# Performance work log

Measured on AMD Instinct MI355X. Metric: run time of the kernel, lower is better.

Reference implementation:

```python
import jax, jax.numpy as jnp
import numpy as np

N = 20000          # nodes (= masked tokens M, node_ids = arange)
E = 320000         # edges
D_H = 256          # hidden_channels
D_Z = 256          # node_channels
D_A = 256          # attn_channels
D_M = 256          # mlp_hidden_channels
V = 512            # predictor vocab size


def setup_inputs() -> dict:
    key = jax.random.key(0)
    ks = jax.random.split(key, 10)

    def lin(k, fan_in, fan_out):
        return jax.random.normal(k, (fan_in, fan_out), jnp.float32) / np.sqrt(fan_in)

    h_mask = jax.random.normal(ks[0], (N, D_H), jnp.float32)
    z = jax.random.normal(ks[1], (N, D_Z), jnp.float32)
    edge_index = jax.random.randint(ks[2], (2, E), 0, N, dtype=jnp.int32)
    node_ids = jnp.arange(N, dtype=jnp.int32)
    # Pairing of (masked token, edge): with node_ids = arange(N), every edge's
    # dst is a masked node, so masked_idx = dst and edge_idx = arange(E).
    masked_idx = edge_index[1]
    edge_idx = jnp.arange(E, dtype=jnp.int32)
    return {
        "h_mask": h_mask,
        "z": z,
        "Wq": lin(ks[3], D_Z, D_A), "bq": jnp.zeros((D_A,), jnp.float32),
        "Wk": lin(ks[4], D_Z, D_A), "bk": jnp.zeros((D_A,), jnp.float32),
        "W1": lin(ks[5], D_Z, D_M), "b1": jnp.zeros((D_M,), jnp.float32),
        "W2": lin(ks[6], D_M, D_H), "b2": jnp.zeros((D_H,), jnp.float32),
        "Wpred": lin(ks[7], D_H, V), "bpred": jnp.zeros((V,), jnp.float32),
        "edge_index": edge_index,
        "node_ids": node_ids,
        "masked_idx": masked_idx,
        "edge_idx": edge_idx,
    }


def reference(h_mask, z, Wq, bq, Wk, bk, W1, b1, W2, b2, Wpred, bpred,
              edge_index, node_ids, masked_idx, edge_idx):
    src = edge_index[0]
    # Node-level projections (N x D), computed once then gathered per pair.
    q = z @ Wq + bq                      # [N, D_A]
    k = z @ Wk + bk                      # [N, D_A]

    center_nodes = jnp.take(node_ids, masked_idx, axis=0)   # [P]
    neighbor_nodes = jnp.take(src, edge_idx, axis=0)        # [P]

    q_i = jnp.take(q, center_nodes, axis=0)                 # [P, D_A]
    k_j = jnp.take(k, neighbor_nodes, axis=0)               # [P, D_A]
    a_ij = jax.nn.sigmoid(jnp.sum(q_i * k_j, axis=-1, keepdims=True))  # [P, 1]

    h_i = jnp.take(h_mask, masked_idx, axis=0)              # [P, D_H]
    z_j = jnp.take(z, neighbor_nodes, axis=0)               # [P, D_Z]
    g_zj = jax.nn.relu(z_j @ W1 + b1) @ W2 + b2             # [P, D_H]

    h_tilde = a_ij * h_i + (1.0 - a_ij) * g_zj              # [P, D_H]
    edge_logits = h_tilde @ Wpred + bpred                   # [P, V]
    return edge_logits, masked_idx
```

## Files before the change

### kernel.cpp

```cpp
#include <hip/hip_runtime.h>
#include <hip/hip_bf16.h>

typedef __attribute__((ext_vector_type(8))) short s16x8;
typedef __attribute__((ext_vector_type(4))) float f32x4;
typedef __attribute__((ext_vector_type(2))) float f32x2;

__device__ inline unsigned int f2bf(float f) {
    union { float f; unsigned int i; } v;
    v.f = f;
    return (v.i + 0x7FFFu + ((v.i >> 16) & 1u)) >> 16;
}
__device__ inline unsigned char f2fp8(float v) {
    const int p = __builtin_amdgcn_cvt_pk_fp8_f32(v, v, 0, false);
    return (unsigned char)(p & 0xFF);
}

__global__ __launch_bounds__(256) void prep_w(
    const float* __restrict__ Wq, const float* __restrict__ Wk,
    const float* __restrict__ W1, const float* __restrict__ W2,
    const float* __restrict__ Wp,
    const float* __restrict__ bq, const float* __restrict__ bk,
    const float* __restrict__ b1,
    unsigned short* __restrict__ Wtqkt, unsigned short* __restrict__ Wt2,
    unsigned short* __restrict__ Wtp, float* __restrict__ bqkt)
{
    const int tid = threadIdx.x;
    int b = blockIdx.x;
    if (b < 1024) {
        const int w = b >> 8;
        const int i = (b & 255) * 256 + tid;
        const int k = i >> 8, j = i & 255;
        const float* W = (w == 0) ? Wq : (w == 1) ? Wk : (w == 2) ? W1 : W2;
        unsigned short* dst = (w == 3) ? Wt2 : (Wtqkt + w * 65536);
        dst[j * 256 + k] = (unsigned short)f2bf(W[i]);
        return;
    }
    b -= 1024;
    if (b < 512) {
        const int i = b * 256 + tid;
        const int k = i >> 9, j = i & 511;
        Wtp[(size_t)j * 256 + k] = (unsigned short)f2bf(Wp[i]);
        return;
    }
    b -= 512;
    {
        const int i = b * 256 + tid;
        bqkt[i] = (i < 256) ? bq[i] : (i < 512) ? bk[i - 256] : b1[i - 512];
    }
}

struct GemmJob {
    const void* A;
    const unsigned short* Wt;
    const float* bias;
    void* out1;
    void* out2;
    int Nout;
    int split;
    int relu_lo, relu_hi;
    int a_f32;
    int fp8_1, fp8_2;
};

__device__ inline void job_store(const GemmJob& J, int row, int col, float v, int M) {
    if (row >= M) return;
    if (J.bias) v += J.bias[col];
    if (col >= J.relu_lo && col < J.relu_hi) v = fmaxf(v, 0.0f);
    const bool lo = (col < J.split);
    void* o = lo ? J.out1 : J.out2;
    const int stride = lo ? J.split : (J.Nout - J.split);
    const int cc = lo ? col : col - J.split;
    const int f8 = lo ? J.fp8_1 : J.fp8_2;
    if (f8) ((unsigned char*)o)[(size_t)row * stride + cc] = f2fp8(v);
    else    ((unsigned short*)o)[(size_t)row * stride + cc] = (unsigned short)f2bf(v);
}

__global__ __launch_bounds__(256) void gemm_multi(
    GemmJob j0, GemmJob j1, int M)
{
    __shared__ __align__(16) char smem[65536];
    char* ldsA = smem;
    char* ldsB = smem + 32768;
    const GemmJob J = (blockIdx.y == 0) ? j0 : j1;

    const int tid  = threadIdx.x;
    const int wid  = tid >> 6, lane = tid & 63;
    const int wr   = wid >> 1, wc = wid & 1;
    const int r0   = blockIdx.x * 64;
    const int swz  = (lane & 7) << 4;

    if (J.a_f32) {
        const float* Af = (const float*)J.A;
        for (int i = tid; i < 2048; i += 256) {
            const int row = i >> 5, off = i & 31;
            const int gr = r0 + row;
            uint4 v = make_uint4(0, 0, 0, 0);
            if (gr < M) {
                const float4 a = *(const float4*)(Af + (size_t)gr * 256 + off * 8);
                const float4 c = *(const float4*)(Af + (size_t)gr * 256 + off * 8 + 4);
                v.x = f2bf(a.x) | (f2bf(a.y) << 16);
                v.y = f2bf(a.z) | (f2bf(a.w) << 16);
                v.z = f2bf(c.x) | (f2bf(c.y) << 16);
                v.w = f2bf(c.z) | (f2bf(c.w) << 16);
            }
            const int b = (row * 512 + off * 16) ^ ((row & 7) << 4);
            *(uint4*)(ldsA + b) = v;
        }
    } else {
        const unsigned short* Ab = (const unsigned short*)J.A;
        for (int i = tid; i < 2048; i += 256) {
            const int row = i >> 5, off = i & 31;
            const int gr = r0 + row;
            uint4 v = make_uint4(0, 0, 0, 0);
            if (gr < M) v = *(const uint4*)(Ab + (size_t)gr * 256 + off * 8);
            const int b = (row * 512 + off * 16) ^ ((row & 7) << 4);
            *(uint4*)(ldsA + b) = v;
        }
    }

    const int ro = lane & 15, ko = (lane >> 4) * 16;
    const int baseA0 = (wr * 32 +  0 + ro) * 512 + ko;
    const int baseA1 = (wr * 32 + 16 + ro) * 512 + ko;
    const int baseB0 = (wc * 32 +  0 + ro) * 512 + ko;
    const int baseB1 = (wc * 32 + 16 + ro) * 512 + ko;

    const int nchunks = J.Nout >> 6;
    for (int c = 0; c < nchunks; ++c) {
        const int j0c = c << 6;
        for (int i = tid; i < 2048; i += 256) {
            const int row = i >> 5, off = i & 31;
            const uint4 v = *(const uint4*)(J.Wt + (size_t)(j0c + row) * 256 + off * 8);
            const int b = (row * 512 + off * 16) ^ ((row & 7) << 4);
            *(uint4*)(ldsB + b) = v;
        }
        __syncthreads();

        f32x4 acc00 = {0,0,0,0}, acc01 = {0,0,0,0}, acc10 = {0,0,0,0}, acc11 = {0,0,0,0};
#pragma unroll
        for (int kk = 0; kk < 8; ++kk) {
            const int kb = kk * 64;
            const s16x8 a0 = *(const s16x8*)(ldsA + ((baseA0 + kb) ^ swz));
            const s16x8 a1 = *(const s16x8*)(ldsA + ((baseA1 + kb) ^ swz));
            const s16x8 b0 = *(const s16x8*)(ldsB + ((baseB0 + kb) ^ swz));
            const s16x8 b1 = *(const s16x8*)(ldsB + ((baseB1 + kb) ^ swz));
            acc00 = __builtin_amdgcn_mfma_f32_16x16x32_bf16(a0, b0, acc00, 0, 0, 0);
            acc01 = __builtin_amdgcn_mfma_f32_16x16x32_bf16(a0, b1, acc01, 0, 0, 0);
            acc10 = __builtin_amdgcn_mfma_f32_16x16x32_bf16(a1, b0, acc10, 0, 0, 0);
            acc11 = __builtin_amdgcn_mfma_f32_16x16x32_bf16(a1, b1, acc11, 0, 0, 0);
        }

        const int colb = j0c + wc * 32;
        const int rb0 = r0 + wr * 32 + (lane >> 4) * 4;
        const int rb1 = rb0 + 16;
#pragma unroll
        for (int r = 0; r < 4; ++r) {
            job_store(J, rb0 + r, colb + ro,      acc00[r], M);
            job_store(J, rb0 + r, colb + 16 + ro, acc01[r], M);
            job_store(J, rb1 + r, colb + ro,      acc10[r], M);
            job_store(J, rb1 + r, colb + 16 + ro, acc11[r], M);
        }
        __syncthreads();
    }
}

__global__ __launch_bounds__(256) void edge_fused(
    const unsigned char* __restrict__ qkb,
    const unsigned char* __restrict__ hp, const unsigned char* __restrict__ gp,
    const float* __restrict__ bpred,
    const int* __restrict__ edge_src, const int* __restrict__ node_ids,
    const int* __restrict__ masked_idx, const int* __restrict__ edge_idx,
    float* __restrict__ out, int P)
{
    const int wave = threadIdx.x >> 6;
    const int lane = threadIdx.x & 63;
    const int e = blockIdx.x * 4 + wave;
    if (e >= P) return;

    const int mi = masked_idx[e];
    const int c  = node_ids[mi];
    const int s  = edge_src[edge_idx[e]];

    const unsigned int qw = *(const unsigned int*)(qkb + (size_t)c * 512 + lane * 4);
    const unsigned int kw = *(const unsigned int*)(qkb + (size_t)s * 512 + 256 + lane * 4);
    const f32x2 q01 = __builtin_amdgcn_cvt_pk_f32_fp8(qw, false);
    const f32x2 q23 = __builtin_amdgcn_cvt_pk_f32_fp8(qw, true);
    const f32x2 k01 = __builtin_amdgcn_cvt_pk_f32_fp8(kw, false);
    const f32x2 k23 = __builtin_amdgcn_cvt_pk_f32_fp8(kw, true);
    float dot = q01.x * k01.x + q01.y * k01.y + q23.x * k23.x + q23.y * k23.y;
#pragma unroll
    for (int off = 32; off; off >>= 1) dot += __shfl_xor(dot, off, 64);

    const float a = 1.0f / (1.0f + expf(-dot));
    const float oma = 1.0f - a;

    const uint2 hv = *(const uint2*)(hp + (size_t)c * 512 + lane * 8);
    const uint2 gv = *(const uint2*)(gp + (size_t)s * 512 + lane * 8);
    const float4 bp0 = *(const float4*)&bpred[lane * 8];
    const float4 bp1 = *(const float4*)&bpred[lane * 8 + 4];

    const f32x2 h0 = __builtin_amdgcn_cvt_pk_f32_fp8(hv.x, false);
    const f32x2 h1 = __builtin_amdgcn_cvt_pk_f32_fp8(hv.x, true);
    const f32x2 h2 = __builtin_amdgcn_cvt_pk_f32_fp8(hv.y, false);
    const f32x2 h3 = __builtin_amdgcn_cvt_pk_f32_fp8(hv.y, true);
    const f32x2 g0 = __builtin_amdgcn_cvt_pk_f32_fp8(gv.x, false);
    const f32x2 g1 = __builtin_amdgcn_cvt_pk_f32_fp8(gv.x, true);
    const f32x2 g2 = __builtin_amdgcn_cvt_pk_f32_fp8(gv.y, false);
    const f32x2 g3 = __builtin_amdgcn_cvt_pk_f32_fp8(gv.y, true);

    f32x4 r0, r1;
    r0[0] = fmaf(a, h0.x, fmaf(oma, g0.x, bp0.x));
    r0[1] = fmaf(a, h0.y, fmaf(oma, g0.y, bp0.y));
    r0[2] = fmaf(a, h1.x, fmaf(oma, g1.x, bp0.z));
    r0[3] = fmaf(a, h1.y, fmaf(oma, g1.y, bp0.w));
    r1[0] = fmaf(a, h2.x, fmaf(oma, g2.x, bp1.x));
    r1[1] = fmaf(a, h2.y, fmaf(oma, g2.y, bp1.y));
    r1[2] = fmaf(a, h3.x, fmaf(oma, g3.x, bp1.z));
    r1[3] = fmaf(a, h3.y, fmaf(oma, g3.y, bp1.w));

    float* dst = &out[(size_t)e * 512 + lane * 8];
    __builtin_nontemporal_store(r0, (f32x4*)dst);
    __builtin_nontemporal_store(r1, (f32x4*)(dst + 4));

    if (lane == 0) {
        __builtin_nontemporal_store((float)mi, &out[(size_t)P * 512 + e]);
    }
}

extern "C" void kernel_launch(void* const* d_in, const int* in_sizes, int n_in,
                              void* d_out, int out_size, void* d_ws, size_t ws_size,
                              hipStream_t stream) {
    const float* h_mask = (const float*)d_in[0];
    const float* z      = (const float*)d_in[1];
    const float* Wq     = (const float*)d_in[2];
    const float* bq     = (const float*)d_in[3];
    const float* Wk     = (const float*)d_in[4];
    const float* bk     = (const float*)d_in[5];
    const float* W1     = (const float*)d_in[6];
    const float* b1     = (const float*)d_in[7];
    const float* W2     = (const float*)d_in[8];
    const float* b2     = (const float*)d_in[9];
    const float* Wpred  = (const float*)d_in[10];
    const float* bpred  = (const float*)d_in[11];
    const int* edge_index = (const int*)d_in[12];
    const int* node_ids   = (const int*)d_in[13];
    const int* masked_idx = (const int*)d_in[14];
    const int* edge_idx   = (const int*)d_in[15];

    const int N = in_sizes[13];
    const int P = in_sizes[14];

    unsigned char*  qkb   = (unsigned char*)d_ws;
    unsigned char*  gpb   = qkb + (size_t)N * 512;
    unsigned char*  hpb   = gpb + (size_t)N * 512;
    unsigned short* tb    = (unsigned short*)(hpb + (size_t)N * 512);
    unsigned short* gb    = tb  + (size_t)N * 256;
    unsigned short* Wtqkt = gb  + (size_t)N * 256;
    unsigned short* Wt2   = Wtqkt + 196608;
    unsigned short* Wtp   = Wt2   + 65536;
    float*          bqkt  = (float*)(Wtp + 131072);

    const dim3 blk(256);
    const int gb64 = (N + 63) / 64;
    const int eb   = (P + 3) / 4;

    prep_w<<<dim3(1024 + 512 + 3), blk, 0, stream>>>(
        Wq, Wk, W1, W2, Wpred, bq, bk, b1, Wtqkt, Wt2, Wtp, bqkt);

    GemmJob a0 = { z,      Wtqkt, bqkt,    qkb, tb,      768, 512, 512, 768, 1, 1, 0 };
    GemmJob a1 = { h_mask, Wtp,   nullptr, hpb, nullptr, 512, 512, 0,   0,   1, 1, 0 };
    gemm_multi<<<dim3(gb64, 2), blk, 0, stream>>>(a0, a1, N);

    GemmJob b0 = { tb, Wt2, b2, gb, nullptr, 256, 256, 0, 0, 0, 0, 0 };
    gemm_multi<<<dim3(gb64, 1), blk, 0, stream>>>(b0, b0, N);

    GemmJob c0 = { gb, Wtp, nullptr, gpb, nullptr, 512, 512, 0, 0, 0, 1, 0 };
    gemm_multi<<<dim3(gb64, 1), blk, 0, stream>>>(c0, c0, N);

    edge_fused<<<dim3(eb), blk, 0, stream>>>(qkb, hpb, gpb, bpred,
                                             edge_index, node_ids, masked_idx, edge_idx,
                                             (float*)d_out, P);
}
```

Before: 319.9 us.

## Counting-sort edges by center node before the fused edge kernel

Adds a counting sort (histogram, single-block scan, atomic scatter) that groups edges by their center node and packs each edge's indices into an int4 record. The edge kernel then walks edges in sorted order, so that q and h rows of the same center node are reused in cache and the index indirection is a single load. The cost is three extra small kernels, including a single-block serial scan over N, plus atomics and a 5 MB index buffer. Output writes still go to the original edge positions, so they become scattered.

```diff
diff --git a/kernel.cpp b/kernel.cpp
--- a/kernel.cpp
+++ b/kernel.cpp
@@ -22,7 +22,8 @@
     const float* __restrict__ bq, const float* __restrict__ bk,
     const float* __restrict__ b1,
     unsigned short* __restrict__ Wtqkt, unsigned short* __restrict__ Wt2,
-    unsigned short* __restrict__ Wtp, float* __restrict__ bqkt)
+    unsigned short* __restrict__ Wtp, float* __restrict__ bqkt,
+    int* __restrict__ counts, int N)
 {
     const int tid = threadIdx.x;
     int b = blockIdx.x;
@@ -43,10 +44,65 @@
         return;
     }
     b -= 512;
+    if (b < 3) {
+        const int i = b * 256 + tid;
+        bqkt[i] = (i < 256) ? bq[i] : (i < 512) ? bk[i - 256] : b1[i - 512];
+        return;
+    }
+    b -= 3;
     {
         const int i = b * 256 + tid;
-        bqkt[i] = (i < 256) ? bq[i] : (i < 512) ? bk[i - 256] : b1[i - 512];
-    }
+        if (i < N) counts[i] = 0;
+    }
+}
+
+__global__ __launch_bounds__(256) void sort_hist(
+    const int* __restrict__ node_ids, const int* __restrict__ masked_idx,
+    int* __restrict__ counts, int P)
+{
+    const int e = blockIdx.x * 256 + threadIdx.x;
+    if (e >= P) return;
+    const int c = node_ids[masked_idx[e]];
+    atomicAdd(&counts[c], 1);
+}
+
+__global__ __launch_bounds__(256) void sort_scan(
+    const int* __restrict__ counts, int* __restrict__ cursor, int N)
+{
+    __shared__ int part[256];
+    const int tid = threadIdx.x;
+    const int chunk = (N + 255) / 256;
+    const int lo = tid * chunk, hi = min(lo + chunk, N);
+
+    int ls = 0;
+    for (int i = lo; i < hi; ++i) ls += counts[i];
+    part[tid] = ls;
+    __syncthreads();
+    for (int off = 1; off < 256; off <<= 1) {
+        int v = (tid >= off) ? part[tid - off] : 0;
+        __syncthreads();
+        part[tid] += v;
+        __syncthreads();
+    }
+    int run = part[tid] - ls;
+    for (int i = lo; i < hi; ++i) {
+        cursor[i] = run;
+        run += counts[i];
+    }
+}
+
+__global__ __launch_bounds__(256) void sort_scatter(
+    const int* __restrict__ edge_src, const int* __restrict__ node_ids,
+    const int* __restrict__ masked_idx, const int* __restrict__ edge_idx,
+    int* __restrict__ cursor, int4* __restrict__ sorted, int P)
+{
+    const int e = blockIdx.x * 256 + threadIdx.x;
+    if (e >= P) return;
+    const int mi = masked_idx[e];
+    const int c  = node_ids[mi];
+    const int s  = edge_src[edge_idx[e]];
+    const int pos = atomicAdd(&cursor[c], 1);
+    sorted[pos] = make_int4(e, mi, c, s);
 }
 
 struct GemmJob {
@@ -163,22 +219,20 @@
     }
 }
 
-__global__ __launch_bounds__(256) void edge_fused(
+__global__ __launch_bounds__(256) void edge_sorted(
+    const int4* __restrict__ sorted,
     const unsigned char* __restrict__ qkb,
     const unsigned char* __restrict__ hp, const unsigned char* __restrict__ gp,
     const float* __restrict__ bpred,
-    const int* __restrict__ edge_src, const int* __restrict__ node_ids,
-    const int* __restrict__ masked_idx, const int* __restrict__ edge_idx,
     float* __restrict__ out, int P)
 {
     const int wave = threadIdx.x >> 6;
     const int lane = threadIdx.x & 63;
-    const int e = blockIdx.x * 4 + wave;
-    if (e >= P) return;
-
-    const int mi = masked_idx[e];
-    const int c  = node_ids[mi];
-    const int s  = edge_src[edge_idx[e]];
+    const int ep = blockIdx.x * 4 + wave;
+    if (ep >= P) return;
+
+    const int4 t = sorted[ep];
+    const int e = t.x, mi = t.y, c = t.z, s = t.w;
 
     const unsigned int qw = *(const unsigned int*)(qkb + (size_t)c * 512 + lane * 4);
     const unsigned int kw = *(const unsigned int*)(qkb + (size_t)s * 512 + 256 + lane * 4);
@@ -258,13 +312,23 @@
     unsigned short* Wt2   = Wtqkt + 196608;
     unsigned short* Wtp   = Wt2   + 65536;
     float*          bqkt  = (float*)(Wtp + 131072);
+    int*            counts = (int*)(bqkt + 768);
+    int*            cursor = counts + N;
+    int4*           sorted = (int4*)(cursor + N);
 
     const dim3 blk(256);
     const int gb64 = (N + 63) / 64;
     const int eb   = (P + 3) / 4;
-
-    prep_w<<<dim3(1024 + 512 + 3), blk, 0, stream>>>(
-        Wq, Wk, W1, W2, Wpred, bq, bk, b1, Wtqkt, Wt2, Wtp, bqkt);
+    const int pb   = (P + 255) / 256;
+    const int nb   = (N + 255) / 256;
+
+    prep_w<<<dim3(1024 + 512 + 3 + nb), blk, 0, stream>>>(
+        Wq, Wk, W1, W2, Wpred, bq, bk, b1, Wtqkt, Wt2, Wtp, bqkt, counts, N);
+
+    sort_hist<<<dim3(pb), blk, 0, stream>>>(node_ids, masked_idx, counts, P);
+    sort_scan<<<dim3(1), blk, 0, stream>>>(counts, cursor, N);
+    sort_scatter<<<dim3(pb), blk, 0, stream>>>(edge_index, node_ids, masked_idx, edge_idx,
+                                               cursor, sorted, P);
 
     GemmJob a0 = { z,      Wtqkt, bqkt,    qkb, tb,      768, 512, 512, 768, 1, 1, 0 };
     GemmJob a1 = { h_mask, Wtp,   nullptr, hpb, nullptr, 512, 512, 0,   0,   1, 1, 0 };
@@ -276,7 +340,6 @@
     GemmJob c0 = { gb, Wtp, nullptr, gpb, nullptr, 512, 512, 0, 0, 0, 1, 0 };
     gemm_multi<<<dim3(gb64, 1), blk, 0, stream>>>(c0, c0, N);
 
-    edge_fused<<<dim3(eb), blk, 0, stream>>>(qkb, hpb, gpb, bpred,
-                                             edge_index, node_ids, masked_idx, edge_idx,
-                                             (float*)d_out, P);
-}
+    edge_sorted<<<dim3(eb), blk, 0, stream>>>(sorted, qkb, hpb, gpb, bpred,
+                                              (float*)d_out, P);
+}
```

New measurement: 457.6 us. +43.0%, slower.

## Fuse node-level GEMM chain into one kernel keeping MLP intermediates in LDS

Applied to the files above, without the earlier changes.

Replaces three gemm_multi launches with a single gemm_fused kernel. For z blocks it computes q/k, then the relu(zW1) tile is held in registers and written back into the LDS A tile. That tile feeds the W2 GEMM and then the Wpred projection, so the bf16 intermediates tb and gb never go to global memory. This removes two launches and the global round-trips of the intermediates, but the z-row blocks now do much more work than the h blocks, which risks load imbalance and higher register pressure.

```diff
diff --git a/kernel.cpp b/kernel.cpp
--- a/kernel.cpp
+++ b/kernel.cpp
@@ -49,48 +49,33 @@
     }
 }
 
-struct GemmJob {
-    const void* A;
-    const unsigned short* Wt;
-    const float* bias;
-    void* out1;
-    void* out2;
-    int Nout;
-    int split;
-    int relu_lo, relu_hi;
-    int a_f32;
-    int fp8_1, fp8_2;
-};
-
-__device__ inline void job_store(const GemmJob& J, int row, int col, float v, int M) {
-    if (row >= M) return;
-    if (J.bias) v += J.bias[col];
-    if (col >= J.relu_lo && col < J.relu_hi) v = fmaxf(v, 0.0f);
-    const bool lo = (col < J.split);
-    void* o = lo ? J.out1 : J.out2;
-    const int stride = lo ? J.split : (J.Nout - J.split);
-    const int cc = lo ? col : col - J.split;
-    const int f8 = lo ? J.fp8_1 : J.fp8_2;
-    if (f8) ((unsigned char*)o)[(size_t)row * stride + cc] = f2fp8(v);
-    else    ((unsigned short*)o)[(size_t)row * stride + cc] = (unsigned short)f2bf(v);
-}
-
-__global__ __launch_bounds__(256) void gemm_multi(
-    GemmJob j0, GemmJob j1, int M)
+__global__ __launch_bounds__(256) void gemm_fused(
+    const float* __restrict__ z, const float* __restrict__ h,
+    const unsigned short* __restrict__ Wtqkt, const unsigned short* __restrict__ Wt2,
+    const unsigned short* __restrict__ Wtp,
+    const float* __restrict__ bqkt, const float* __restrict__ b2,
+    unsigned char* __restrict__ qkb, unsigned char* __restrict__ hpb,
+    unsigned char* __restrict__ gpb, int M)
 {
     __shared__ __align__(16) char smem[65536];
     char* ldsA = smem;
     char* ldsB = smem + 32768;
-    const GemmJob J = (blockIdx.y == 0) ? j0 : j1;
 
     const int tid  = threadIdx.x;
     const int wid  = tid >> 6, lane = tid & 63;
     const int wr   = wid >> 1, wc = wid & 1;
     const int r0   = blockIdx.x * 64;
     const int swz  = (lane & 7) << 4;
-
-    if (J.a_f32) {
-        const float* Af = (const float*)J.A;
+    const int ro   = lane & 15, ko = (lane >> 4) * 16;
+    const int lr0  = wr * 32 + (lane >> 4) * 4;
+    const int baseA0 = (wr * 32 +  0 + ro) * 512 + ko;
+    const int baseA1 = (wr * 32 + 16 + ro) * 512 + ko;
+    const int baseB0 = (wc * 32 +  0 + ro) * 512 + ko;
+    const int baseB1 = (wc * 32 + 16 + ro) * 512 + ko;
+
+    f32x4 a00, a01, a10, a11;
+
+    auto stageAf = [&](const float* Af) {
         for (int i = tid; i < 2048; i += 256) {
             const int row = i >> 5, off = i & 31;
             const int gr = r0 + row;
@@ -103,64 +88,112 @@
                 v.z = f2bf(c.x) | (f2bf(c.y) << 16);
                 v.w = f2bf(c.z) | (f2bf(c.w) << 16);
             }
-            const int b = (row * 512 + off * 16) ^ ((row & 7) << 4);
-            *(uint4*)(ldsA + b) = v;
-        }
-    } else {
-        const unsigned short* Ab = (const unsigned short*)J.A;
+            *(uint4*)(ldsA + ((row * 512 + off * 16) ^ ((row & 7) << 4))) = v;
+        }
+    };
+
+    auto chunk = [&](const unsigned short* Wt, int rowbase) {
         for (int i = tid; i < 2048; i += 256) {
             const int row = i >> 5, off = i & 31;
-            const int gr = r0 + row;
-            uint4 v = make_uint4(0, 0, 0, 0);
-            if (gr < M) v = *(const uint4*)(Ab + (size_t)gr * 256 + off * 8);
-            const int b = (row * 512 + off * 16) ^ ((row & 7) << 4);
-            *(uint4*)(ldsA + b) = v;
-        }
-    }
-
-    const int ro = lane & 15, ko = (lane >> 4) * 16;
-    const int baseA0 = (wr * 32 +  0 + ro) * 512 + ko;
-    const int baseA1 = (wr * 32 + 16 + ro) * 512 + ko;
-    const int baseB0 = (wc * 32 +  0 + ro) * 512 + ko;
-    const int baseB1 = (wc * 32 + 16 + ro) * 512 + ko;
-
-    const int nchunks = J.Nout >> 6;
-    for (int c = 0; c < nchunks; ++c) {
-        const int j0c = c << 6;
-        for (int i = tid; i < 2048; i += 256) {
-            const int row = i >> 5, off = i & 31;
-            const uint4 v = *(const uint4*)(J.Wt + (size_t)(j0c + row) * 256 + off * 8);
-            const int b = (row * 512 + off * 16) ^ ((row & 7) << 4);
-            *(uint4*)(ldsB + b) = v;
+            const uint4 v = *(const uint4*)(Wt + (size_t)(rowbase + row) * 256 + off * 8);
+            *(uint4*)(ldsB + ((row * 512 + off * 16) ^ ((row & 7) << 4))) = v;
         }
         __syncthreads();
-
-        f32x4 acc00 = {0,0,0,0}, acc01 = {0,0,0,0}, acc10 = {0,0,0,0}, acc11 = {0,0,0,0};
+        a00 = (f32x4){0,0,0,0}; a01 = (f32x4){0,0,0,0};
+        a10 = (f32x4){0,0,0,0}; a11 = (f32x4){0,0,0,0};
 #pragma unroll
         for (int kk = 0; kk < 8; ++kk) {
             const int kb = kk * 64;
-            const s16x8 a0 = *(const s16x8*)(ldsA + ((baseA0 + kb) ^ swz));
-            const s16x8 a1 = *(const s16x8*)(ldsA + ((baseA1 + kb) ^ swz));
-            const s16x8 b0 = *(const s16x8*)(ldsB + ((baseB0 + kb) ^ swz));
-            const s16x8 b1 = *(const s16x8*)(ldsB + ((baseB1 + kb) ^ swz));
-            acc00 = __builtin_amdgcn_mfma_f32_16x16x32_bf16(a0, b0, acc00, 0, 0, 0);
-            acc01 = __builtin_amdgcn_mfma_f32_16x16x32_bf16(a0, b1, acc01, 0, 0, 0);
-            acc10 = __builtin_amdgcn_mfma_f32_16x16x32_bf16(a1, b0, acc10, 0, 0, 0);
-            acc11 = __builtin_amdgcn_mfma_f32_16x16x32_bf16(a1, b1, acc11, 0, 0, 0);
-        }
-
-        const int colb = j0c + wc * 32;
-        const int rb0 = r0 + wr * 32 + (lane >> 4) * 4;
-        const int rb1 = rb0 + 16;
+            const s16x8 x0 = *(const s16x8*)(ldsA + ((baseA0 + kb) ^ swz));
+            const s16x8 x1 = *(const s16x8*)(ldsA + ((baseA1 + kb) ^ swz));
+            const s16x8 y0 = *(const s16x8*)(ldsB + ((baseB0 + kb) ^ swz));
+            const s16x8 y1 = *(const s16x8*)(ldsB + ((baseB1 + kb) ^ swz));
+            a00 = __builtin_amdgcn_mfma_f32_16x16x32_bf16(x0, y0, a00, 0, 0, 0);
+            a01 = __builtin_amdgcn_mfma_f32_16x16x32_bf16(x0, y1, a01, 0, 0, 0);
+            a10 = __builtin_amdgcn_mfma_f32_16x16x32_bf16(x1, y0, a10, 0, 0, 0);
+            a11 = __builtin_amdgcn_mfma_f32_16x16x32_bf16(x1, y1, a11, 0, 0, 0);
+        }
+    };
+
+    auto store_fp8 = [&](unsigned char* outb, int colbase, const float* bias) {
+        const int cb = colbase + wc * 32;
+        const float bs0 = bias ? bias[cb + ro] : 0.0f;
+        const float bs1 = bias ? bias[cb + 16 + ro] : 0.0f;
+        const int gr0 = r0 + lr0, gr1 = gr0 + 16;
 #pragma unroll
         for (int r = 0; r < 4; ++r) {
-            job_store(J, rb0 + r, colb + ro,      acc00[r], M);
-            job_store(J, rb0 + r, colb + 16 + ro, acc01[r], M);
-            job_store(J, rb1 + r, colb + ro,      acc10[r], M);
-            job_store(J, rb1 + r, colb + 16 + ro, acc11[r], M);
+            if (gr0 + r < M) {
+                outb[(size_t)(gr0 + r) * 512 + cb + ro]      = f2fp8(a00[r] + bs0);
+                outb[(size_t)(gr0 + r) * 512 + cb + 16 + ro] = f2fp8(a01[r] + bs1);
+            }
+            if (gr1 + r < M) {
+                outb[(size_t)(gr1 + r) * 512 + cb + ro]      = f2fp8(a10[r] + bs0);
+                outb[(size_t)(gr1 + r) * 512 + cb + 16 + ro] = f2fp8(a11[r] + bs1);
+            }
         }
         __syncthreads();
-    }
+    };
+
+    auto frag_to_ldsA = [&](const unsigned int* treg) {
+#pragma unroll
+        for (int tc = 0; tc < 4; ++tc) {
+            const int cb = tc * 64 + wc * 32;
+#pragma unroll
+            for (int r = 0; r < 4; ++r) {
+                const unsigned int w0 = treg[tc * 8 + r * 2];
+                const unsigned int w1 = treg[tc * 8 + r * 2 + 1];
+                const int row0 = lr0 + r, row1 = row0 + 16;
+                *(unsigned short*)(ldsA + ((row0 * 512 + (cb + ro) * 2)      ^ ((row0 & 7) << 4))) = (unsigned short)(w0 & 0xFFFFu);
+                *(unsigned short*)(ldsA + ((row0 * 512 + (cb + 16 + ro) * 2) ^ ((row0 & 7) << 4))) = (unsigned short)(w0 >> 16);
+                *(unsigned short*)(ldsA + ((row1 * 512 + (cb + ro) * 2)      ^ ((row1 & 7) << 4))) = (unsigned short)(w1 & 0xFFFFu);
+                *(unsigned short*)(ldsA + ((row1 * 512 + (cb + 16 + ro) * 2) ^ ((row1 & 7) << 4))) = (unsigned short)(w1 >> 16);
+            }
+        }
+    };
+
+    if (blockIdx.y == 1) {
+        stageAf(h);
+        for (int c = 0; c < 8; ++c) { chunk(Wtp, c * 64); store_fp8(hpb, c * 64, nullptr); }
+        return;
+    }
+
+    stageAf(z);
+    for (int c = 0; c < 8; ++c) { chunk(Wtqkt, c * 64); store_fp8(qkb, c * 64, bqkt); }
+
+    unsigned int treg[32];
+#pragma unroll
+    for (int tc = 0; tc < 4; ++tc) {
+        chunk(Wtqkt, 512 + tc * 64);
+        const int cb = tc * 64 + wc * 32;
+        const float bs0 = bqkt[512 + cb + ro];
+        const float bs1 = bqkt[512 + cb + 16 + ro];
+#pragma unroll
+        for (int r = 0; r < 4; ++r) {
+            treg[tc * 8 + r * 2]     = f2bf(fmaxf(a00[r] + bs0, 0.0f)) | (f2bf(fmaxf(a01[r] + bs1, 0.0f)) << 16);
+            treg[tc * 8 + r * 2 + 1] = f2bf(fmaxf(a10[r] + bs0, 0.0f)) | (f2bf(fmaxf(a11[r] + bs1, 0.0f)) << 16);
+        }
+        __syncthreads();
+    }
+    frag_to_ldsA(treg);
+    __syncthreads();
+
+#pragma unroll
+    for (int gc = 0; gc < 4; ++gc) {
+        chunk(Wt2, gc * 64);
+        const int cb = gc * 64 + wc * 32;
+        const float bs0 = b2[cb + ro];
+        const float bs1 = b2[cb + 16 + ro];
+#pragma unroll
+        for (int r = 0; r < 4; ++r) {
+            treg[gc * 8 + r * 2]     = f2bf(a00[r] + bs0) | (f2bf(a01[r] + bs1) << 16);
+            treg[gc * 8 + r * 2 + 1] = f2bf(a10[r] + bs0) | (f2bf(a11[r] + bs1) << 16);
+        }
+        __syncthreads();
+    }
+    frag_to_ldsA(treg);
+    __syncthreads();
+
+    for (int c = 0; c < 8; ++c) { chunk(Wtp, c * 64); store_fp8(gpb, c * 64, nullptr); }
 }
 
 __global__ __launch_bounds__(256) void edge_fused(
@@ -252,9 +285,7 @@
     unsigned char*  qkb   = (unsigned char*)d_ws;
     unsigned char*  gpb   = qkb + (size_t)N * 512;
     unsigned char*  hpb   = gpb + (size_t)N * 512;
-    unsigned short* tb    = (unsigned short*)(hpb + (size_t)N * 512);
-    unsigned short* gb    = tb  + (size_t)N * 256;
-    unsigned short* Wtqkt = gb  + (size_t)N * 256;
+    unsigned short* Wtqkt = (unsigned short*)(hpb + (size_t)N * 512);
     unsigned short* Wt2   = Wtqkt + 196608;
     unsigned short* Wtp   = Wt2   + 65536;
     float*          bqkt  = (float*)(Wtp + 131072);
@@ -266,15 +297,8 @@
     prep_w<<<dim3(1024 + 512 + 3), blk, 0, stream>>>(
         Wq, Wk, W1, W2, Wpred, bq, bk, b1, Wtqkt, Wt2, Wtp, bqkt);
 
-    GemmJob a0 = { z,      Wtqkt, bqkt,    qkb, tb,      768, 512, 512, 768, 1, 1, 0 };
-    GemmJob a1 = { h_mask, Wtp,   nullptr, hpb, nullptr, 512, 512, 0,   0,   1, 1, 0 };
-    gemm_multi<<<dim3(gb64, 2), blk, 0, stream>>>(a0, a1, N);
-
-    GemmJob b0 = { tb, Wt2, b2, gb, nullptr, 256, 256, 0, 0, 0, 0, 0 };
-    gemm_multi<<<dim3(gb64, 1), blk, 0, stream>>>(b0, b0, N);
-
-    GemmJob c0 = { gb, Wtp, nullptr, gpb, nullptr, 512, 512, 0, 0, 0, 1, 0 };
-    gemm_multi<<<dim3(gb64, 1), blk, 0, stream>>>(c0, c0, N);
+    gemm_fused<<<dim3(gb64, 2), blk, 0, stream>>>(
+        z, h_mask, Wtqkt, Wt2, Wtp, bqkt, b2, qkb, hpb, gpb, N);
 
     edge_fused<<<dim3(eb), blk, 0, stream>>>(qkb, hpb, gpb, bpred,
                                              edge_index, node_ids, masked_idx, edge_idx,
```

Measured after the change: 316.0 us. Within noise of the previous version (-1.2%).
